# Kernel optimization log

Hardware: AMD Instinct MI355X
Metric: run time of the kernel (lower is better)

The kernel has to match this reference:

```python
import jax, jax.numpy as jnp
import numpy as np

HEADS = 4


def setup_inputs() -> dict:
    key = jax.random.key(0)
    ks = jax.random.split(key, 8)
    B, N, P, C, H = 8, 325, 64, 64, 64
    s = 0.02
    return {
        "x": jax.random.normal(ks[0], (B, N, P, C), dtype=jnp.float32),
        "adjacency": jax.random.randint(ks[1], (N, N), 0, 2, dtype=jnp.int32),
        "W_in": jax.random.normal(ks[2], (C, H), dtype=jnp.float32) * s,
        "b_in": jnp.zeros((H,), jnp.float32),
        "in_proj_w": jax.random.normal(ks[3], (3 * H, H), dtype=jnp.float32) * s,
        "in_proj_b": jnp.zeros((3 * H,), jnp.float32),
        "out_w": jax.random.normal(ks[4], (H, H), dtype=jnp.float32) * s,
        "out_b": jnp.zeros((H,), jnp.float32),
        "W_out": jax.random.normal(ks[5], (H, C), dtype=jnp.float32) * s,
        "b_out": jnp.zeros((C,), jnp.float32),
    }


def reference(x, adjacency, W_in, b_in, in_proj_w, in_proj_b, out_w, out_b, W_out, b_out):
    B, N, P, C = x.shape
    H = W_in.shape[1]
    hd = H // HEADS

    # attention mask: adjacency with forced self-loops; 0 where edge, -inf otherwise
    adj = adjacency.astype(jnp.float32)
    adj = adj.at[jnp.diag_indices(N)].set(1.0)
    mask = jnp.where(adj > 0, 0.0, -jnp.inf)  # (N, N)

    # input projection: (B, N, P, C) -> (B, N, P, H)
    h = x @ W_in + b_in
    # faithful to torch .view on contiguous (B, N, P, H) tensor (raw reshape, not transpose)
    h = h.reshape(B * P, N, H)

    # in-projection (torch packs q,k,v weights as (3H, H))
    q = h @ in_proj_w[:H].T + in_proj_b[:H]
    k = h @ in_proj_w[H:2 * H].T + in_proj_b[H:2 * H]
    v = h @ in_proj_w[2 * H:].T + in_proj_b[2 * H:]

    def split_heads(t):  # (BP, N, H) -> (BP, HEADS, N, hd)
        return t.reshape(B * P, N, HEADS, hd).transpose(0, 2, 1, 3)

    q, k, v = split_heads(q), split_heads(k), split_heads(v)

    scores = jnp.einsum('bhqd,bhkd->bhqk', q, k) / jnp.sqrt(jnp.float32(hd)) + mask
    attn = jax.nn.softmax(scores, axis=-1)
    o = jnp.einsum('bhqk,bhkd->bhqd', attn, v)
    o = o.transpose(0, 2, 1, 3).reshape(B * P, N, H)
    o = o @ out_w.T + out_b  # MHA out_proj

    y = o @ W_out.T + b_out  # output projection back to C
    y = y.reshape(B, P, N, C).transpose(0, 2, 1, 3)  # (B, N, P, C)
    return jax.nn.gelu(y, approximate=False)
```

## Files before the change

kernel.cpp:

```cpp
#include <hip/hip_runtime.h>
#include <hip/hip_bf16.h>
#include <math.h>

#define NN 325
#define NROWS (8*325*64)
#define RELEM ((size_t)NROWS * 64)
#define NTILES (NROWS/16)
#define QSC 0.36067376022224085f
#define QT2 11

using bf16x8 = __attribute__((ext_vector_type(8))) short;
using f32x4  = __attribute__((ext_vector_type(4))) float;
using f32x16 = __attribute__((ext_vector_type(16))) float;
using u32x2  = __attribute__((ext_vector_type(2))) unsigned;

union BF8 { bf16x8 v; unsigned u[4]; };

static __device__ inline short f2bf(float f) {
    unsigned u = __float_as_uint(f);
    unsigned r = (u + 0x7fffu + ((u >> 16) & 1u)) >> 16;
    return (short)r;
}
static __device__ inline unsigned pk2(float a, float b) {
    __hip_bfloat162 h = __float22bfloat162_rn(make_float2(a, b));
    union { __hip_bfloat162 h; unsigned u; } c; c.h = h; return c.u;
}
static __device__ inline void gload16(const void* g, void* l) {
    __builtin_amdgcn_global_load_lds(
        (const __attribute__((address_space(1))) void*)g,
        (__attribute__((address_space(3))) void*)l, 16, 0, 0);
}

__global__ __launch_bounds__(256) void kprep(const float* __restrict__ Win,
                                             const float* __restrict__ ipw,
                                             const float* __restrict__ outw,
                                             const float* __restrict__ wout,
                                             short* __restrict__ Wp) {
    int idx = blockIdx.x * 256 + threadIdx.x;
    if (idx >= 24576) return;
    int mat = idx >> 12, ft = (idx >> 9) & 7, lane = (idx >> 3) & 63, j = idx & 7;
    int m = (ft >> 1) * 16 + (lane & 15);
    int k = (ft & 1) * 32 + (lane >> 4) * 8 + j;
    float w;
    if (mat == 0)      w = Win[k * 64 + m];
    else if (mat <= 3) w = ipw[((mat - 1) * 64 + m) * 64 + k];
    else if (mat == 4) w = outw[m * 64 + k];
    else               w = wout[m * 64 + k];
    short hi = f2bf(w);
    float hif = __uint_as_float(((unsigned)(unsigned short)hi) << 16);
    short lo = f2bf(w - hif);
    int base = mat * 8192 + ft * 1024 + lane * 8 + j;
    Wp[base] = hi;
    Wp[base + 512] = lo;
}

__global__ __launch_bounds__(256) void kbias(const int* __restrict__ adj,
                                             float* __restrict__ Sb) {
    int idx = blockIdx.x * 256 + threadIdx.x;
    if (idx >= QT2 * QT2 * 64) return;
    int lane = idx & 63, kt2 = (idx >> 6) % QT2, qt2 = idx / (QT2 * 64);
    int l31 = lane & 31, hi = lane >> 5;
    int q = qt2 * 32 + l31;
#pragma unroll
    for (int g = 0; g < 4; ++g) {
        float v[4];
#pragma unroll
        for (int rr = 0; rr < 4; ++rr) {
            int r = g * 4 + rr;
            int key = kt2 * 32 + (r & 3) + 8 * (r >> 2) + 4 * hi;
            bool valid = (q < NN) && (key < NN) &&
                         (q == key || adj[q * NN + key] != 0);
            v[rr] = valid ? 0.0f : -INFINITY;
        }
        float4 o; o.x = v[0]; o.y = v[1]; o.z = v[2]; o.w = v[3];
        *(float4*)(Sb + (size_t)idx * 16 + g * 4) = o;
    }
}

__global__ __launch_bounds__(256, 2) void kqkv(const float* __restrict__ X,
                                               const float* __restrict__ bin,
                                               const float* __restrict__ ipb,
                                               const short* __restrict__ Wp,
                                               short* __restrict__ Q,
                                               short* __restrict__ Kb,
                                               short* __restrict__ Vb) {
    __shared__ short wl[32768];
    __shared__ __align__(16) short hf[4][2048];
    int tid = threadIdx.x;
    {
        const uint4* src = (const uint4*)Wp;
        uint4* dst = (uint4*)wl;
#pragma unroll
        for (int i = 0; i < 16; ++i) dst[tid + i * 256] = src[tid + i * 256];
    }
    __syncthreads();

    int wave = tid >> 6, lane = tid & 63, quad = lane >> 4, l15 = lane & 15;
    short* hfw = hf[wave];
    char* hfb = (char*)hfw;

    int srow = lane >> 4;
    int sslot = lane & 15;
    int stride = gridDim.x * 4;

    int tile = blockIdx.x * 4 + wave;
    {
        const char* xt = (const char*)X + (size_t)tile * 4096;
#pragma unroll
        for (int i = 0; i < 4; ++i) {
            int r = i * 4 + srow;
            gload16(xt + r * 256 + ((sslot ^ r) << 4), hfb + i * 1024 + lane * 16);
        }
    }

    while (tile < NTILES) {
        asm volatile("s_waitcnt vmcnt(0)" ::: "memory");
        __builtin_amdgcn_sched_barrier(0);

        BF8 xbh[2], xbl[2];
#pragma unroll
        for (int kc = 0; kc < 2; ++kc) {
            float e[8];
#pragma unroll
            for (int h = 0; h < 2; ++h) {
                int slot = (kc * 8 + quad * 2 + h) ^ l15;
                float4 v = *(const float4*)(hfb + l15 * 256 + slot * 16);
                e[h * 4 + 0] = v.x; e[h * 4 + 1] = v.y;
                e[h * 4 + 2] = v.z; e[h * 4 + 3] = v.w;
            }
            unsigned hh[4], ll[4];
#pragma unroll
            for (int p = 0; p < 4; ++p) {
                hh[p] = pk2(e[2 * p], e[2 * p + 1]);
                float f0 = __uint_as_float(hh[p] << 16);
                float f1 = __uint_as_float(hh[p] & 0xFFFF0000u);
                ll[p] = pk2(e[2 * p] - f0, e[2 * p + 1] - f1);
            }
#pragma unroll
            for (int p = 0; p < 4; ++p) { xbh[kc].u[p] = hh[p]; xbl[kc].u[p] = ll[p]; }
        }

#pragma unroll
        for (int mt = 0; mt < 4; ++mt) {
            float4 bv = *(const float4*)(bin + mt * 16 + quad * 4);
            f32x4 acc = {bv.x, bv.y, bv.z, bv.w};
#pragma unroll
            for (int kc = 0; kc < 2; ++kc) {
                const short* ap = wl + (mt * 2 + kc) * 1024 + lane * 8;
                bf16x8 ah = *(const bf16x8*)ap;
                bf16x8 al = *(const bf16x8*)(ap + 512);
                acc = __builtin_amdgcn_mfma_f32_16x16x32_bf16(ah, xbh[kc].v, acc, 0, 0, 0);
                acc = __builtin_amdgcn_mfma_f32_16x16x32_bf16(ah, xbl[kc].v, acc, 0, 0, 0);
                acc = __builtin_amdgcn_mfma_f32_16x16x32_bf16(al, xbh[kc].v, acc, 0, 0, 0);
            }
            int kc2 = mt >> 1;
            int lane2 = ((mt & 1) * 2 + (quad >> 1)) * 16 + l15;
            int jb = (quad & 1) * 4;
            unsigned u01 = pk2(acc[0], acc[1]), u23 = pk2(acc[2], acc[3]);
            uint2 wh; wh.x = u01; wh.y = u23;
            *(uint2*)(hfw + kc2 * 1024 + lane2 * 8 + jb) = wh;
            float f0 = __uint_as_float(u01 << 16), f1 = __uint_as_float(u01 & 0xFFFF0000u);
            float f2 = __uint_as_float(u23 << 16), f3 = __uint_as_float(u23 & 0xFFFF0000u);
            uint2 wlo; wlo.x = pk2(acc[0] - f0, acc[1] - f1);
            wlo.y = pk2(acc[2] - f2, acc[3] - f3);
            *(uint2*)(hfw + kc2 * 1024 + 512 + lane2 * 8 + jb) = wlo;
        }

        BF8 hbh[2], hbl[2];
#pragma unroll
        for (int kc = 0; kc < 2; ++kc) {
            hbh[kc].v = *(const bf16x8*)(hfw + kc * 1024 + lane * 8);
            hbl[kc].v = *(const bf16x8*)(hfw + kc * 1024 + 512 + lane * 8);
        }

        asm volatile("s_waitcnt lgkmcnt(0)" ::: "memory");
        __builtin_amdgcn_sched_barrier(0);

        int nt = tile + stride;
        if (nt < NTILES) {
            const char* xt = (const char*)X + (size_t)nt * 4096;
#pragma unroll
            for (int i = 0; i < 4; ++i) {
                int r = i * 4 + srow;
                gload16(xt + r * 256 + ((sslot ^ r) << 4), hfb + i * 1024 + lane * 16);
            }
        }

        size_t row = (size_t)tile * 16 + l15;
#pragma unroll
        for (int t = 0; t < 3; ++t) {
            short* Out = (t == 0) ? Q : (t == 1) ? Kb : Vb;
            float sc = (t == 0) ? QSC : 1.0f;
#pragma unroll
            for (int mt = 0; mt < 4; ++mt) {
                float4 bv = *(const float4*)(ipb + t * 64 + mt * 16 + quad * 4);
                f32x4 acc = {bv.x, bv.y, bv.z, bv.w};
#pragma unroll
                for (int kc = 0; kc < 2; ++kc) {
                    const short* ap = wl + (1 + t) * 8192 + (mt * 2 + kc) * 1024 + lane * 8;
                    bf16x8 ah = *(const bf16x8*)ap;
                    bf16x8 al = *(const bf16x8*)(ap + 512);
                    acc = __builtin_amdgcn_mfma_f32_16x16x32_bf16(ah, hbh[kc].v, acc, 0, 0, 0);
                    acc = __builtin_amdgcn_mfma_f32_16x16x32_bf16(ah, hbl[kc].v, acc, 0, 0, 0);
                    acc = __builtin_amdgcn_mfma_f32_16x16x32_bf16(al, hbh[kc].v, acc, 0, 0, 0);
                }
                uint2 st; st.x = pk2(acc[0] * sc, acc[1] * sc);
                st.y = pk2(acc[2] * sc, acc[3] * sc);
                *(uint2*)(Out + ((size_t)mt * NROWS + row) * 16 + quad * 4) = st;
            }
        }
        tile = nt;
    }
}

__global__ __launch_bounds__(256) void kattn(const short* __restrict__ Q,
                                             const short* __restrict__ K,
                                             const short* __restrict__ V,
                                             const float* __restrict__ Sb,
                                             float* __restrict__ O) {
    __shared__ __align__(16) short ks[352 * 24];
    __shared__ __align__(16) short vsT[17 * 360];

    int b = blockIdx.x;
    int xcd = b & 7, slot = b >> 3;
    int i = (slot >> 2) * 8 + xcd, head = slot & 3;
    const short* Kb  = K + ((size_t)head * NROWS + (size_t)i * NN) * 16;
    const short* Vbp = V + ((size_t)head * NROWS + (size_t)i * NN) * 16;
    const short* Qb  = Q + ((size_t)head * NROWS + (size_t)i * NN) * 16;
    float*       Ob  = O + ((size_t)head * NROWS + (size_t)i * NN) * 16;
    int tid = threadIdx.x;

    for (int kn = tid; kn < 352; kn += 256) {
        bf16x8 ka = {0,0,0,0,0,0,0,0}, kb = {0,0,0,0,0,0,0,0};
        bf16x8 va = {0,0,0,0,0,0,0,0}, vb = {0,0,0,0,0,0,0,0};
        if (kn < NN) {
            ka = *(const bf16x8*)(Kb + (size_t)kn * 16);
            kb = *(const bf16x8*)(Kb + (size_t)kn * 16 + 8);
            va = *(const bf16x8*)(Vbp + (size_t)kn * 16);
            vb = *(const bf16x8*)(Vbp + (size_t)kn * 16 + 8);
        }
        *(bf16x8*)(ks + kn * 24) = ka;
        *(bf16x8*)(ks + kn * 24 + 8) = kb;
#pragma unroll
        for (int d = 0; d < 8; ++d) vsT[d * 360 + kn] = va[d];
#pragma unroll
        for (int d = 0; d < 8; ++d) vsT[(8 + d) * 360 + kn] = vb[d];
    }
    for (int kn = tid; kn < 360; kn += 256) vsT[16 * 360 + kn] = (short)0x3F80;
    __syncthreads();

    int wave = tid >> 6, lane = tid & 63;
    int l31 = lane & 31, hi = lane >> 5, l15 = lane & 15;
    const short* vrow = vsT + (l31 < 16 ? l31 : 16) * 360 + hi * 8;
    const short* krow = ks + hi * 8;

    for (int qt2 = wave; qt2 < QT2; qt2 += 4) {
        int qr = qt2 * 32 + l31; if (qr > NN - 1) qr = NN - 1;
        bf16x8 bq = *(const bf16x8*)(Qb + (size_t)qr * 16 + hi * 8);
        f32x16 acc = {};
        const float* sbp = Sb + ((size_t)(qt2 * QT2) * 64 + lane) * 16;

        bf16x8 ak = *(const bf16x8*)(krow + (size_t)l31 * 24);
        f32x16 cb = *(const f32x16*)(sbp);

        for (int kt2 = 0; kt2 < QT2; ++kt2) {
            f32x16 s = __builtin_amdgcn_mfma_f32_32x32x16_bf16(ak, bq, cb, 0, 0, 0);

            int nk = kt2 + 1; nk = (nk == QT2) ? 0 : nk;
            ak = *(const bf16x8*)(krow + (size_t)(nk * 32 + l31) * 24);
            cb = *(const f32x16*)(sbp + (size_t)nk * 1024);
            bf16x8 v0 = *(const bf16x8*)(vrow + kt2 * 32);
            bf16x8 v1 = *(const bf16x8*)(vrow + kt2 * 32 + 16);

            float p[16];
#pragma unroll
            for (int r = 0; r < 16; ++r) p[r] = __builtin_amdgcn_exp2f(s[r]);

            unsigned w0 = pk2(p[0],  p[1]),  w1 = pk2(p[2],  p[3]);
            unsigned w2 = pk2(p[4],  p[5]),  w3 = pk2(p[6],  p[7]);
            unsigned w4 = pk2(p[8],  p[9]),  w5 = pk2(p[10], p[11]);
            unsigned w6 = pk2(p[12], p[13]), w7 = pk2(p[14], p[15]);
            u32x2 s02 = __builtin_amdgcn_permlane32_swap(w0, w2, false, false);
            u32x2 s13 = __builtin_amdgcn_permlane32_swap(w1, w3, false, false);
            u32x2 s46 = __builtin_amdgcn_permlane32_swap(w4, w6, false, false);
            u32x2 s57 = __builtin_amdgcn_permlane32_swap(w5, w7, false, false);
            BF8 pa0, pa1;
            pa0.u[0] = s02[0]; pa0.u[1] = s13[0]; pa0.u[2] = s02[1]; pa0.u[3] = s13[1];
            pa1.u[0] = s46[0]; pa1.u[1] = s57[0]; pa1.u[2] = s46[1]; pa1.u[3] = s57[1];

            acc = __builtin_amdgcn_mfma_f32_32x32x16_bf16(pa0.v, v0, acc, 0, 0, 0);
            acc = __builtin_amdgcn_mfma_f32_32x32x16_bf16(pa1.v, v1, acc, 0, 0, 0);
        }

#pragma unroll
        for (int r = 0; r < 16; ++r) {
            float den = __shfl_xor(acc[r], 16, 64);
            float inv = __builtin_amdgcn_rcpf(den);
            inv = inv * (2.0f - den * inv);
            int qn = qt2 * 32 + (r & 3) + 8 * (r >> 2) + 4 * hi;
            if (l31 < 16 && qn < NN)
                Ob[(size_t)qn * 16 + l15] = acc[r] * inv;
        }
    }
}

__global__ __launch_bounds__(256, 2) void kfinal(const float* __restrict__ Ob,
                                                 const float* __restrict__ outb,
                                                 const float* __restrict__ boutv,
                                                 const short* __restrict__ Wp,
                                                 float* __restrict__ Yout) {
    __shared__ short wl[16384];
    __shared__ __align__(16) short hf[4][2048];
    int tid = threadIdx.x;
    {
        const uint4* src = (const uint4*)Wp;
        uint4* dst = (uint4*)wl;
#pragma unroll
        for (int i = 0; i < 8; ++i) dst[tid + i * 256] = src[4096 + tid + i * 256];
    }
    __syncthreads();

    int wave = tid >> 6, lane = tid & 63, quad = lane >> 4, l15 = lane & 15;
    short* hfw = hf[wave];

    for (int tile = blockIdx.x * 4 + wave; tile < NTILES; tile += gridDim.x * 4) {
        size_t row = (size_t)tile * 16 + l15;

        BF8 obh[2], obl[2];
#pragma unroll
        for (int kc = 0; kc < 2; ++kc) {
            const float* xp = Ob + ((size_t)(kc * 2 + (quad >> 1)) * NROWS + row) * 16
                              + (quad & 1) * 8;
            float4 v0 = *(const float4*)xp;
            float4 v1 = *(const float4*)(xp + 4);
            float e[8] = {v0.x, v0.y, v0.z, v0.w, v1.x, v1.y, v1.z, v1.w};
            unsigned hh[4], ll[4];
#pragma unroll
            for (int p = 0; p < 4; ++p) {
                hh[p] = pk2(e[2 * p], e[2 * p + 1]);
                float f0 = __uint_as_float(hh[p] << 16);
                float f1 = __uint_as_float(hh[p] & 0xFFFF0000u);
                ll[p] = pk2(e[2 * p] - f0, e[2 * p + 1] - f1);
            }
#pragma unroll
            for (int p = 0; p < 4; ++p) { obh[kc].u[p] = hh[p]; obl[kc].u[p] = ll[p]; }
        }

#pragma unroll
        for (int mt = 0; mt < 4; ++mt) {
            float4 bv = *(const float4*)(outb + mt * 16 + quad * 4);
            f32x4 acc = {bv.x, bv.y, bv.z, bv.w};
#pragma unroll
            for (int kc = 0; kc < 2; ++kc) {
                const short* ap = wl + (mt * 2 + kc) * 1024 + lane * 8;
                bf16x8 ah = *(const bf16x8*)ap;
                bf16x8 al = *(const bf16x8*)(ap + 512);
                acc = __builtin_amdgcn_mfma_f32_16x16x32_bf16(ah, obh[kc].v, acc, 0, 0, 0);
                acc = __builtin_amdgcn_mfma_f32_16x16x32_bf16(ah, obl[kc].v, acc, 0, 0, 0);
                acc = __builtin_amdgcn_mfma_f32_16x16x32_bf16(al, obh[kc].v, acc, 0, 0, 0);
            }
            int kc2 = mt >> 1;
            int lane2 = ((mt & 1) * 2 + (quad >> 1)) * 16 + l15;
            int jb = (quad & 1) * 4;
            unsigned u01 = pk2(acc[0], acc[1]), u23 = pk2(acc[2], acc[3]);
            uint2 wh; wh.x = u01; wh.y = u23;
            *(uint2*)(hfw + kc2 * 1024 + lane2 * 8 + jb) = wh;
            float f0 = __uint_as_float(u01 << 16), f1 = __uint_as_float(u01 & 0xFFFF0000u);
            float f2 = __uint_as_float(u23 << 16), f3 = __uint_as_float(u23 & 0xFFFF0000u);
            uint2 wlo; wlo.x = pk2(acc[0] - f0, acc[1] - f1);
            wlo.y = pk2(acc[2] - f2, acc[3] - f3);
            *(uint2*)(hfw + kc2 * 1024 + 512 + lane2 * 8 + jb) = wlo;
        }

        BF8 tbh[2], tbl[2];
#pragma unroll
        for (int kc = 0; kc < 2; ++kc) {
            tbh[kc].v = *(const bf16x8*)(hfw + kc * 1024 + lane * 8);
            tbl[kc].v = *(const bf16x8*)(hfw + kc * 1024 + 512 + lane * 8);
        }

        float* yf = (float*)hfw;
#pragma unroll
        for (int mt = 0; mt < 4; ++mt) {
            float4 bv = *(const float4*)(boutv + mt * 16 + quad * 4);
            f32x4 acc = {bv.x, bv.y, bv.z, bv.w};
#pragma unroll
            for (int kc = 0; kc < 2; ++kc) {
                const short* ap = wl + 8192 + (mt * 2 + kc) * 1024 + lane * 8;
                bf16x8 ah = *(const bf16x8*)ap;
                bf16x8 al = *(const bf16x8*)(ap + 512);
                acc = __builtin_amdgcn_mfma_f32_16x16x32_bf16(ah, tbh[kc].v, acc, 0, 0, 0);
                acc = __builtin_amdgcn_mfma_f32_16x16x32_bf16(ah, tbl[kc].v, acc, 0, 0, 0);
                acc = __builtin_amdgcn_mfma_f32_16x16x32_bf16(al, tbh[kc].v, acc, 0, 0, 0);
            }
            float4 yv;
            yv.x = 0.5f * acc[0] * (1.0f + erff(acc[0] * 0.70710678118654752f));
            yv.y = 0.5f * acc[1] * (1.0f + erff(acc[1] * 0.70710678118654752f));
            yv.z = 0.5f * acc[2] * (1.0f + erff(acc[2] * 0.70710678118654752f));
            yv.w = 0.5f * acc[3] * (1.0f + erff(acc[3] * 0.70710678118654752f));
            int cblk = mt * 4 + quad;
            int pos = cblk ^ (l15 & 7);
            *(float4*)(yf + l15 * 64 + pos * 4) = yv;
        }
#pragma unroll
        for (int s = 0; s < 4; ++s) {
            int rr = s * 4 + (lane >> 4);
            float4 w = *(const float4*)(yf + rr * 64 + ((l15 ^ (rr & 7)) * 4));
            unsigned rw2 = (unsigned)(tile * 16 + rr);
            unsigned ii2 = rw2 / NN, n2 = rw2 - ii2 * NN;
            size_t ob2 = (((size_t)(ii2 >> 6) * NN + n2) * 64 + (ii2 & 63)) * 64;
            *(float4*)(Yout + ob2 + l15 * 4) = w;
        }
    }
}

extern "C" void kernel_launch(void* const* d_in, const int* in_sizes, int n_in,
                              void* d_out, int out_size, void* d_ws, size_t ws_size,
                              hipStream_t stream) {
    const float* x    = (const float*)d_in[0];
    const int*   adj  = (const int*)  d_in[1];
    const float* W_in = (const float*)d_in[2];
    const float* b_in = (const float*)d_in[3];
    const float* ipw  = (const float*)d_in[4];
    const float* ipb  = (const float*)d_in[5];
    const float* outw = (const float*)d_in[6];
    const float* outb = (const float*)d_in[7];
    const float* wout = (const float*)d_in[8];
    const float* bout = (const float*)d_in[9];
    float* out = (float*)d_out;

    char* wsb = (char*)d_ws;
    short* bufQ = (short*)(wsb);
    short* bufK = (short*)(wsb + 2 * RELEM);
    short* bufV = (short*)(wsb + 4 * RELEM);
    float* bufO = (float*)(wsb + 6 * RELEM);
    short* Wp   = (short*)(wsb + 10 * RELEM);
    float* Sb   = (float*)(wsb + 10 * RELEM + 98304);

    hipLaunchKernelGGL(kprep,  dim3(96),  dim3(256), 0, stream, W_in, ipw, outw, wout, Wp);
    hipLaunchKernelGGL(kbias,  dim3(31),  dim3(256), 0, stream, adj, Sb);
    hipLaunchKernelGGL(kqkv,   dim3(512), dim3(256), 0, stream,
                       x, b_in, ipb, Wp, bufQ, bufK, bufV);
    hipLaunchKernelGGL(kattn,  dim3(512 * 4), dim3(256), 0, stream,
                       bufQ, bufK, bufV, Sb, bufO);
    hipLaunchKernelGGL(kfinal, dim3(768), dim3(256), 0, stream,
                       bufO, outb, bout, Wp, out);
}
```

Before: 226.0 us.

## Replace float mask bias with bitmask and read weights from global instead of LDS

The attention mask changes from a precomputed float bias tile (16 floats per lane per tile pair) to a 32-bit bitmask per lane. Each exp2 result is ANDed with a sign-extended mask bit, so the score MFMA accumulates from zero instead of loading the bias. The qkv and final kernels stop staging the packed weights into shared memory and read them directly from global/L2. This frees LDS, so the occupancy hint rises to 4 and the grids grow to 1024 blocks. The trade-off is more global weight reads per MFMA against less LDS staging and less mask bandwidth in attention.

New measurement: 325.6 us. 44.0% more time.

```diff
diff --git a/kernel.cpp b/kernel.cpp
--- a/kernel.cpp
+++ b/kernel.cpp
@@ -29,6 +29,14 @@
     __builtin_amdgcn_global_load_lds(
         (const __attribute__((address_space(1))) void*)g,
         (__attribute__((address_space(3))) void*)l, 16, 0, 0);
+}
+static __device__ inline float maskp(float p, unsigned mw, int r) {
+#if __has_builtin(__builtin_amdgcn_sbfe)
+    unsigned keep = (unsigned)__builtin_amdgcn_sbfe((int)mw, (unsigned)r, 1u);
+#else
+    unsigned keep = (unsigned)((int)(mw << (31 - r)) >> 31);
+#endif
+    return __uint_as_float(__float_as_uint(p) & keep);
 }
 
 __global__ __launch_bounds__(256) void kprep(const float* __restrict__ Win,
@@ -55,46 +63,32 @@
 }
 
 __global__ __launch_bounds__(256) void kbias(const int* __restrict__ adj,
-                                             float* __restrict__ Sb) {
+                                             unsigned* __restrict__ Mg) {
     int idx = blockIdx.x * 256 + threadIdx.x;
     if (idx >= QT2 * QT2 * 64) return;
     int lane = idx & 63, kt2 = (idx >> 6) % QT2, qt2 = idx / (QT2 * 64);
     int l31 = lane & 31, hi = lane >> 5;
     int q = qt2 * 32 + l31;
-#pragma unroll
-    for (int g = 0; g < 4; ++g) {
-        float v[4];
-#pragma unroll
-        for (int rr = 0; rr < 4; ++rr) {
-            int r = g * 4 + rr;
-            int key = kt2 * 32 + (r & 3) + 8 * (r >> 2) + 4 * hi;
-            bool valid = (q < NN) && (key < NN) &&
-                         (q == key || adj[q * NN + key] != 0);
-            v[rr] = valid ? 0.0f : -INFINITY;
-        }
-        float4 o; o.x = v[0]; o.y = v[1]; o.z = v[2]; o.w = v[3];
-        *(float4*)(Sb + (size_t)idx * 16 + g * 4) = o;
-    }
-}
-
-__global__ __launch_bounds__(256, 2) void kqkv(const float* __restrict__ X,
+    unsigned m = 0;
+#pragma unroll
+    for (int r = 0; r < 16; ++r) {
+        int key = kt2 * 32 + (r & 3) + 8 * (r >> 2) + 4 * hi;
+        bool valid = (q < NN) && (key < NN) &&
+                     (q == key || adj[q * NN + key] != 0);
+        m |= (valid ? 1u : 0u) << r;
+    }
+    Mg[idx] = m;
+}
+
+__global__ __launch_bounds__(256, 4) void kqkv(const float* __restrict__ X,
                                                const float* __restrict__ bin,
                                                const float* __restrict__ ipb,
                                                const short* __restrict__ Wp,
                                                short* __restrict__ Q,
                                                short* __restrict__ Kb,
                                                short* __restrict__ Vb) {
-    __shared__ short wl[32768];
     __shared__ __align__(16) short hf[4][2048];
     int tid = threadIdx.x;
-    {
-        const uint4* src = (const uint4*)Wp;
-        uint4* dst = (uint4*)wl;
-#pragma unroll
-        for (int i = 0; i < 16; ++i) dst[tid + i * 256] = src[tid + i * 256];
-    }
-    __syncthreads();
-
     int wave = tid >> 6, lane = tid & 63, quad = lane >> 4, l15 = lane & 15;
     short* hfw = hf[wave];
     char* hfb = (char*)hfw;
@@ -104,7 +98,7 @@
     int stride = gridDim.x * 4;
 
     int tile = blockIdx.x * 4 + wave;
-    {
+    if (tile < NTILES) {
         const char* xt = (const char*)X + (size_t)tile * 4096;
 #pragma unroll
         for (int i = 0; i < 4; ++i) {
@@ -146,7 +140,7 @@
             f32x4 acc = {bv.x, bv.y, bv.z, bv.w};
 #pragma unroll
             for (int kc = 0; kc < 2; ++kc) {
-                const short* ap = wl + (mt * 2 + kc) * 1024 + lane * 8;
+                const short* ap = Wp + (mt * 2 + kc) * 1024 + lane * 8;
                 bf16x8 ah = *(const bf16x8*)ap;
                 bf16x8 al = *(const bf16x8*)(ap + 512);
                 acc = __builtin_amdgcn_mfma_f32_16x16x32_bf16(ah, xbh[kc].v, acc, 0, 0, 0);
@@ -197,7 +191,7 @@
                 f32x4 acc = {bv.x, bv.y, bv.z, bv.w};
 #pragma unroll
                 for (int kc = 0; kc < 2; ++kc) {
-                    const short* ap = wl + (1 + t) * 8192 + (mt * 2 + kc) * 1024 + lane * 8;
+                    const short* ap = Wp + (1 + t) * 8192 + (mt * 2 + kc) * 1024 + lane * 8;
                     bf16x8 ah = *(const bf16x8*)ap;
                     bf16x8 al = *(const bf16x8*)(ap + 512);
                     acc = __builtin_amdgcn_mfma_f32_16x16x32_bf16(ah, hbh[kc].v, acc, 0, 0, 0);
@@ -216,7 +210,7 @@
 __global__ __launch_bounds__(256) void kattn(const short* __restrict__ Q,
                                              const short* __restrict__ K,
                                              const short* __restrict__ V,
-                                             const float* __restrict__ Sb,
+                                             const unsigned* __restrict__ Mg,
                                              float* __restrict__ O) {
     __shared__ __align__(16) short ks[352 * 24];
     __shared__ __align__(16) short vsT[17 * 360];
@@ -254,27 +248,30 @@
     const short* vrow = vsT + (l31 < 16 ? l31 : 16) * 360 + hi * 8;
     const short* krow = ks + hi * 8;
 
+    f32x16 cz = {};
+
     for (int qt2 = wave; qt2 < QT2; qt2 += 4) {
         int qr = qt2 * 32 + l31; if (qr > NN - 1) qr = NN - 1;
         bf16x8 bq = *(const bf16x8*)(Qb + (size_t)qr * 16 + hi * 8);
         f32x16 acc = {};
-        const float* sbp = Sb + ((size_t)(qt2 * QT2) * 64 + lane) * 16;
+        const unsigned* mgp = Mg + (size_t)(qt2 * QT2) * 64 + lane;
 
         bf16x8 ak = *(const bf16x8*)(krow + (size_t)l31 * 24);
-        f32x16 cb = *(const f32x16*)(sbp);
+        unsigned mw = mgp[0];
 
         for (int kt2 = 0; kt2 < QT2; ++kt2) {
-            f32x16 s = __builtin_amdgcn_mfma_f32_32x32x16_bf16(ak, bq, cb, 0, 0, 0);
+            f32x16 s = __builtin_amdgcn_mfma_f32_32x32x16_bf16(ak, bq, cz, 0, 0, 0);
 
             int nk = kt2 + 1; nk = (nk == QT2) ? 0 : nk;
             ak = *(const bf16x8*)(krow + (size_t)(nk * 32 + l31) * 24);
-            cb = *(const f32x16*)(sbp + (size_t)nk * 1024);
+            unsigned mwn = mgp[nk * 64];
             bf16x8 v0 = *(const bf16x8*)(vrow + kt2 * 32);
             bf16x8 v1 = *(const bf16x8*)(vrow + kt2 * 32 + 16);
 
             float p[16];
 #pragma unroll
-            for (int r = 0; r < 16; ++r) p[r] = __builtin_amdgcn_exp2f(s[r]);
+            for (int r = 0; r < 16; ++r)
+                p[r] = maskp(__builtin_amdgcn_exp2f(s[r]), mw, r);
 
             unsigned w0 = pk2(p[0],  p[1]),  w1 = pk2(p[2],  p[3]);
             unsigned w2 = pk2(p[4],  p[5]),  w3 = pk2(p[6],  p[7]);
@@ -290,6 +287,7 @@
 
             acc = __builtin_amdgcn_mfma_f32_32x32x16_bf16(pa0.v, v0, acc, 0, 0, 0);
             acc = __builtin_amdgcn_mfma_f32_32x32x16_bf16(pa1.v, v1, acc, 0, 0, 0);
+            mw = mwn;
         }
 
 #pragma unroll
@@ -304,22 +302,13 @@
     }
 }
 
-__global__ __launch_bounds__(256, 2) void kfinal(const float* __restrict__ Ob,
+__global__ __launch_bounds__(256, 4) void kfinal(const float* __restrict__ Ob,
                                                  const float* __restrict__ outb,
                                                  const float* __restrict__ boutv,
                                                  const short* __restrict__ Wp,
                                                  float* __restrict__ Yout) {
-    __shared__ short wl[16384];
     __shared__ __align__(16) short hf[4][2048];
     int tid = threadIdx.x;
-    {
-        const uint4* src = (const uint4*)Wp;
-        uint4* dst = (uint4*)wl;
-#pragma unroll
-        for (int i = 0; i < 8; ++i) dst[tid + i * 256] = src[4096 + tid + i * 256];
-    }
-    __syncthreads();
-
     int wave = tid >> 6, lane = tid & 63, quad = lane >> 4, l15 = lane & 15;
     short* hfw = hf[wave];
 
@@ -352,7 +341,7 @@
             f32x4 acc = {bv.x, bv.y, bv.z, bv.w};
 #pragma unroll
             for (int kc = 0; kc < 2; ++kc) {
-                const short* ap = wl + (mt * 2 + kc) * 1024 + lane * 8;
+                const short* ap = Wp + 32768 + (mt * 2 + kc) * 1024 + lane * 8;
                 bf16x8 ah = *(const bf16x8*)ap;
                 bf16x8 al = *(const bf16x8*)(ap + 512);
                 acc = __builtin_amdgcn_mfma_f32_16x16x32_bf16(ah, obh[kc].v, acc, 0, 0, 0);
@@ -386,7 +375,7 @@
             f32x4 acc = {bv.x, bv.y, bv.z, bv.w};
 #pragma unroll
             for (int kc = 0; kc < 2; ++kc) {
-                const short* ap = wl + 8192 + (mt * 2 + kc) * 1024 + lane * 8;
+                const short* ap = Wp + 40960 + (mt * 2 + kc) * 1024 + lane * 8;
                 bf16x8 ah = *(const bf16x8*)ap;
                 bf16x8 al = *(const bf16x8*)(ap + 512);
                 acc = __builtin_amdgcn_mfma_f32_16x16x32_bf16(ah, tbh[kc].v, acc, 0, 0, 0);
@@ -435,14 +424,14 @@
     short* bufV = (short*)(wsb + 4 * RELEM);
     float* bufO = (float*)(wsb + 6 * RELEM);
     short* Wp   = (short*)(wsb + 10 * RELEM);
-    float* Sb   = (float*)(wsb + 10 * RELEM + 98304);
-
-    hipLaunchKernelGGL(kprep,  dim3(96),  dim3(256), 0, stream, W_in, ipw, outw, wout, Wp);
-    hipLaunchKernelGGL(kbias,  dim3(31),  dim3(256), 0, stream, adj, Sb);
-    hipLaunchKernelGGL(kqkv,   dim3(512), dim3(256), 0, stream,
+    unsigned* Mg = (unsigned*)(wsb + 10 * RELEM + 98304);
+
+    hipLaunchKernelGGL(kprep,  dim3(96),   dim3(256), 0, stream, W_in, ipw, outw, wout, Wp);
+    hipLaunchKernelGGL(kbias,  dim3(31),   dim3(256), 0, stream, adj, Mg);
+    hipLaunchKernelGGL(kqkv,   dim3(1024), dim3(256), 0, stream,
                        x, b_in, ipb, Wp, bufQ, bufK, bufV);
     hipLaunchKernelGGL(kattn,  dim3(512 * 4), dim3(256), 0, stream,
-                       bufQ, bufK, bufV, Sb, bufO);
-    hipLaunchKernelGGL(kfinal, dim3(768), dim3(256), 0, stream,
+                       bufQ, bufK, bufV, Mg, bufO);
+    hipLaunchKernelGGL(kfinal, dim3(1024), dim3(256), 0, stream,
                        bufO, outb, bout, Wp, out);
 }
```

## Replace float attention bias with packed bitmask and read K directly from global

Applied to the files above, without the earlier changes.

The precomputed -inf/0 float bias tile per lane (16 floats) becomes a 16-bit validity mask in one uint. The score MFMA now starts from zero, and masked probabilities are cleared after exp2 with a bitwise AND. This cuts mask traffic per tile from 64 bytes to 4 bytes per lane. The K staging into LDS is also removed, and each wave loads K fragments straight from global memory, saving LDS space and a staging pass at the cost of repeated global/L2 reads of K across waves.

After: 223.6 us. Within noise of the previous version (-1.1%).

```diff
diff --git a/kernel.cpp b/kernel.cpp
--- a/kernel.cpp
+++ b/kernel.cpp
@@ -29,6 +29,10 @@
     __builtin_amdgcn_global_load_lds(
         (const __attribute__((address_space(1))) void*)g,
         (__attribute__((address_space(3))) void*)l, 16, 0, 0);
+}
+static __device__ inline float maskp(float p, unsigned mw, int r) {
+    unsigned keep = (unsigned)((int)(mw << (31 - r)) >> 31);
+    return __uint_as_float(__float_as_uint(p) & keep);
 }
 
 __global__ __launch_bounds__(256) void kprep(const float* __restrict__ Win,
@@ -55,26 +59,21 @@
 }
 
 __global__ __launch_bounds__(256) void kbias(const int* __restrict__ adj,
-                                             float* __restrict__ Sb) {
+                                             unsigned* __restrict__ Mg) {
     int idx = blockIdx.x * 256 + threadIdx.x;
     if (idx >= QT2 * QT2 * 64) return;
     int lane = idx & 63, kt2 = (idx >> 6) % QT2, qt2 = idx / (QT2 * 64);
     int l31 = lane & 31, hi = lane >> 5;
     int q = qt2 * 32 + l31;
-#pragma unroll
-    for (int g = 0; g < 4; ++g) {
-        float v[4];
-#pragma unroll
-        for (int rr = 0; rr < 4; ++rr) {
-            int r = g * 4 + rr;
-            int key = kt2 * 32 + (r & 3) + 8 * (r >> 2) + 4 * hi;
-            bool valid = (q < NN) && (key < NN) &&
-                         (q == key || adj[q * NN + key] != 0);
-            v[rr] = valid ? 0.0f : -INFINITY;
-        }
-        float4 o; o.x = v[0]; o.y = v[1]; o.z = v[2]; o.w = v[3];
-        *(float4*)(Sb + (size_t)idx * 16 + g * 4) = o;
-    }
+    unsigned m = 0;
+#pragma unroll
+    for (int r = 0; r < 16; ++r) {
+        int key = kt2 * 32 + (r & 3) + 8 * (r >> 2) + 4 * hi;
+        bool valid = (q < NN) && (key < NN) &&
+                     (q == key || adj[q * NN + key] != 0);
+        m |= (valid ? 1u : 0u) << r;
+    }
+    Mg[idx] = m;
 }
 
 __global__ __launch_bounds__(256, 2) void kqkv(const float* __restrict__ X,
@@ -216,31 +215,25 @@
 __global__ __launch_bounds__(256) void kattn(const short* __restrict__ Q,
                                              const short* __restrict__ K,
                                              const short* __restrict__ V,
-                                             const float* __restrict__ Sb,
+                                             const unsigned* __restrict__ Mg,
                                              float* __restrict__ O) {
-    __shared__ __align__(16) short ks[352 * 24];
     __shared__ __align__(16) short vsT[17 * 360];
 
     int b = blockIdx.x;
     int xcd = b & 7, slot = b >> 3;
     int i = (slot >> 2) * 8 + xcd, head = slot & 3;
-    const short* Kb  = K + ((size_t)head * NROWS + (size_t)i * NN) * 16;
+    const short* Kg  = K + ((size_t)head * NROWS + (size_t)i * NN) * 16;
     const short* Vbp = V + ((size_t)head * NROWS + (size_t)i * NN) * 16;
     const short* Qb  = Q + ((size_t)head * NROWS + (size_t)i * NN) * 16;
     float*       Ob  = O + ((size_t)head * NROWS + (size_t)i * NN) * 16;
     int tid = threadIdx.x;
 
     for (int kn = tid; kn < 352; kn += 256) {
-        bf16x8 ka = {0,0,0,0,0,0,0,0}, kb = {0,0,0,0,0,0,0,0};
         bf16x8 va = {0,0,0,0,0,0,0,0}, vb = {0,0,0,0,0,0,0,0};
         if (kn < NN) {
-            ka = *(const bf16x8*)(Kb + (size_t)kn * 16);
-            kb = *(const bf16x8*)(Kb + (size_t)kn * 16 + 8);
             va = *(const bf16x8*)(Vbp + (size_t)kn * 16);
             vb = *(const bf16x8*)(Vbp + (size_t)kn * 16 + 8);
         }
-        *(bf16x8*)(ks + kn * 24) = ka;
-        *(bf16x8*)(ks + kn * 24 + 8) = kb;
 #pragma unroll
         for (int d = 0; d < 8; ++d) vsT[d * 360 + kn] = va[d];
 #pragma unroll
@@ -252,29 +245,32 @@
     int wave = tid >> 6, lane = tid & 63;
     int l31 = lane & 31, hi = lane >> 5, l15 = lane & 15;
     const short* vrow = vsT + (l31 < 16 ? l31 : 16) * 360 + hi * 8;
-    const short* krow = ks + hi * 8;
+    const short* kgl = Kg + (size_t)l31 * 16 + hi * 8;
+
+    f32x16 cz = {};
 
     for (int qt2 = wave; qt2 < QT2; qt2 += 4) {
         int qr = qt2 * 32 + l31; if (qr > NN - 1) qr = NN - 1;
         bf16x8 bq = *(const bf16x8*)(Qb + (size_t)qr * 16 + hi * 8);
         f32x16 acc = {};
-        const float* sbp = Sb + ((size_t)(qt2 * QT2) * 64 + lane) * 16;
-
-        bf16x8 ak = *(const bf16x8*)(krow + (size_t)l31 * 24);
-        f32x16 cb = *(const f32x16*)(sbp);
+        const unsigned* mgp = Mg + (size_t)(qt2 * QT2) * 64 + lane;
+
+        bf16x8 ak = *(const bf16x8*)(kgl);
+        unsigned mw = mgp[0];
 
         for (int kt2 = 0; kt2 < QT2; ++kt2) {
-            f32x16 s = __builtin_amdgcn_mfma_f32_32x32x16_bf16(ak, bq, cb, 0, 0, 0);
+            f32x16 s = __builtin_amdgcn_mfma_f32_32x32x16_bf16(ak, bq, cz, 0, 0, 0);
 
             int nk = kt2 + 1; nk = (nk == QT2) ? 0 : nk;
-            ak = *(const bf16x8*)(krow + (size_t)(nk * 32 + l31) * 24);
-            cb = *(const f32x16*)(sbp + (size_t)nk * 1024);
+            ak = *(const bf16x8*)(kgl + (size_t)nk * 512);
+            unsigned mwn = mgp[nk * 64];
             bf16x8 v0 = *(const bf16x8*)(vrow + kt2 * 32);
             bf16x8 v1 = *(const bf16x8*)(vrow + kt2 * 32 + 16);
 
             float p[16];
 #pragma unroll
-            for (int r = 0; r < 16; ++r) p[r] = __builtin_amdgcn_exp2f(s[r]);
+            for (int r = 0; r < 16; ++r)
+                p[r] = maskp(__builtin_amdgcn_exp2f(s[r]), mw, r);
 
             unsigned w0 = pk2(p[0],  p[1]),  w1 = pk2(p[2],  p[3]);
             unsigned w2 = pk2(p[4],  p[5]),  w3 = pk2(p[6],  p[7]);
@@ -290,6 +286,7 @@
 
             acc = __builtin_amdgcn_mfma_f32_32x32x16_bf16(pa0.v, v0, acc, 0, 0, 0);
             acc = __builtin_amdgcn_mfma_f32_32x32x16_bf16(pa1.v, v1, acc, 0, 0, 0);
+            mw = mwn;
         }
 
 #pragma unroll
@@ -435,14 +432,14 @@
     short* bufV = (short*)(wsb + 4 * RELEM);
     float* bufO = (float*)(wsb + 6 * RELEM);
     short* Wp   = (short*)(wsb + 10 * RELEM);
-    float* Sb   = (float*)(wsb + 10 * RELEM + 98304);
+    unsigned* Mg = (unsigned*)(wsb + 10 * RELEM + 98304);
 
     hipLaunchKernelGGL(kprep,  dim3(96),  dim3(256), 0, stream, W_in, ipw, outw, wout, Wp);
-    hipLaunchKernelGGL(kbias,  dim3(31),  dim3(256), 0, stream, adj, Sb);
+    hipLaunchKernelGGL(kbias,  dim3(31),  dim3(256), 0, stream, adj, Mg);
     hipLaunchKernelGGL(kqkv,   dim3(512), dim3(256), 0, stream,
                        x, b_in, ipb, Wp, bufQ, bufK, bufV);
     hipLaunchKernelGGL(kattn,  dim3(512 * 4), dim3(256), 0, stream,
-                       bufQ, bufK, bufV, Sb, bufO);
+                       bufQ, bufK, bufV, Mg, bufO);
     hipLaunchKernelGGL(kfinal, dim3(768), dim3(256), 0, stream,
                        bufO, outb, bout, Wp, out);
 }
```
